# Kernel optimization log

Hardware: AMD Instinct MI355X
Metric: run time of the kernel (lower is better)

Reference implementation:

```python
import jax, jax.numpy as jnp
import numpy as np

IN_FEATURES = 4096
OUT_FEATURES = 4096
N_GROUPS = 32
GROUP_SIZE = IN_FEATURES // N_GROUPS  # 128


def setup_inputs() -> dict:
    key = jax.random.key(0)
    k_x, k_qw, k_s, k_zp, k_b = jax.random.split(key, 5)
    x = jax.random.normal(k_x, (2, 2048, IN_FEATURES), dtype=jnp.float32)
    # 4-bit GPTQ quantized weight values in [0, 16)
    qweight_int = jax.random.randint(k_qw, (IN_FEATURES, OUT_FEATURES), 0, 16, dtype=jnp.int32)
    scales = jax.random.uniform(k_s, (N_GROUPS, OUT_FEATURES), dtype=jnp.float32, minval=0.001, maxval=0.02)
    zero_points = jax.random.randint(k_zp, (N_GROUPS, OUT_FEATURES), 0, 16, dtype=jnp.int32)
    # standard (non-permuted) g_idx: group index per input channel
    g_idx = (jnp.arange(IN_FEATURES, dtype=jnp.int32) // GROUP_SIZE).astype(jnp.int32)
    bias = jax.random.normal(k_b, (OUT_FEATURES,), dtype=jnp.float32)
    return {"x": x, "qweight_int": qweight_int, "scales": scales,
            "zero_points": zero_points, "g_idx": g_idx, "bias": bias}


def reference(x, qweight_int, scales, zero_points, g_idx, bias):
    dtype = x.dtype
    gi = g_idx.astype(jnp.int32)
    # dequantize: W[i, o] = scales[g_idx[i], o] * (q[i, o] - zp[g_idx[i], o])
    qw = qweight_int.astype(dtype)                       # [in, out]
    zp = zero_points.astype(dtype)[gi]                   # [in, out] via gather
    sc = scales.astype(dtype)[gi]                        # [in, out] via gather
    weight = sc * (qw - zp)                              # [in, out]
    out_shape = x.shape[:-1] + (qweight_int.shape[1],)
    x2d = x.reshape(-1, x.shape[-1])                     # [tokens, in]
    out = (x2d @ weight).reshape(out_shape)              # [b, s, out]
    out = out + bias.astype(dtype)
    return out
```

## Files before the change

### kernel.cpp

```cpp
#include <hip/hip_runtime.h>
#include <hip/hip_bf16.h>

typedef int  int4v  __attribute__((ext_vector_type(4)));
typedef int  int16v __attribute__((ext_vector_type(16)));

#define M_DIM 4096
#define N_DIM 4096
#define K_DIM 4096
#define NG 32
#define GS 128

__global__ void prep_kernel(const float* __restrict__ x,
                            signed char* __restrict__ xq,
                            float* __restrict__ sx,
                            const int* __restrict__ qw,
                            const int* __restrict__ zps,
                            signed char* __restrict__ wq) {
    const int tid = threadIdx.x;
    if (blockIdx.x < 4096) {
        __shared__ float red[4];
        __shared__ float inv_s;
        const int m = blockIdx.x;
        const float4* xr = reinterpret_cast<const float4*>(x + (long)m * K_DIM);
        float4 v[4];
        float amax = 0.f;
#pragma unroll
        for (int j = 0; j < 4; ++j) {
            v[j] = xr[tid * 4 + j];
            amax = fmaxf(amax, fmaxf(fmaxf(fabsf(v[j].x), fabsf(v[j].y)),
                                     fmaxf(fabsf(v[j].z), fabsf(v[j].w))));
        }
#pragma unroll
        for (int off = 32; off >= 1; off >>= 1)
            amax = fmaxf(amax, __shfl_xor(amax, off));
        if ((tid & 63) == 0) red[tid >> 6] = amax;
        __syncthreads();
        if (tid == 0) {
            float a = fmaxf(fmaxf(red[0], red[1]), fmaxf(red[2], red[3]));
            sx[m] = a * (1.f / 127.f);
            inv_s = (a > 0.f) ? 127.f / a : 0.f;
        }
        __syncthreads();
        const float inv = inv_s;
        unsigned p[4];
#pragma unroll
        for (int j = 0; j < 4; ++j) {
            int a0 = __float2int_rn(v[j].x * inv);
            int a1 = __float2int_rn(v[j].y * inv);
            int a2 = __float2int_rn(v[j].z * inv);
            int a3 = __float2int_rn(v[j].w * inv);
            p[j] = (a0 & 255) | ((a1 & 255) << 8) | ((a2 & 255) << 16) | ((a3 & 255) << 24);
        }
        *reinterpret_cast<uint4*>(xq + (long)m * K_DIM + tid * 16) =
            make_uint4(p[0], p[1], p[2], p[3]);
        return;
    }
    __shared__ signed char lt[128 * 32];
    const int bx = blockIdx.x - 4096;
    const int n0 = (bx & 127) * 32;
    const int k0 = (bx >> 7) * 128;
    const int g  = bx >> 7;
    const int kl = tid >> 1;
    const int h  = tid & 1;
    int4 qv[4], zv[4];
#pragma unroll
    for (int c = 0; c < 4; ++c) {
        qv[c] = *reinterpret_cast<const int4*>(&qw[(long)(k0 + kl) * N_DIM + n0 + h * 16 + c * 4]);
        zv[c] = *reinterpret_cast<const int4*>(&zps[(long)g * N_DIM + n0 + h * 16 + c * 4]);
    }
    {
        const int swz = ((kl >> 3) & 7) << 2;
        int* ltw = reinterpret_cast<int*>(lt);
#pragma unroll
        for (int c = 0; c < 4; ++c) {
            unsigned d = (unsigned)((qv[c].x - zv[c].x) & 255)
                       | ((unsigned)((qv[c].y - zv[c].y) & 255) << 8)
                       | ((unsigned)((qv[c].z - zv[c].z) & 255) << 16)
                       | ((unsigned)((qv[c].w - zv[c].w) & 255) << 24);
            ltw[(kl * 32 + ((h * 16 + c * 4) ^ swz)) >> 2] = d;
        }
    }
    __syncthreads();
    const int nl = tid >> 3;
    const int kq = tid & 7;
    unsigned acc[4] = {0u, 0u, 0u, 0u};
#pragma unroll
    for (int j = 0; j < 16; ++j) {
        const int kr = kq * 16 + j;
        unsigned by = (unsigned char)lt[kr * 32 + (nl ^ (((kr >> 3) & 7) << 2))];
        acc[j >> 2] |= by << (8 * (j & 3));
    }
    *reinterpret_cast<uint4*>(wq + (long)(n0 + nl) * K_DIM + k0 + kq * 16) =
        make_uint4(acc[0], acc[1], acc[2], acc[3]);
}

#define BM 128
#define BN 256
#define BK 64
#define NSTEP (K_DIM / BK)

__device__ __forceinline__ void async_ld16(const signed char* g, const signed char* l) {
    __builtin_amdgcn_global_load_lds(
        (const __attribute__((address_space(1))) void*)g,
        (__attribute__((address_space(3))) void*)l, 16, 0, 0);
}

__device__ __forceinline__ int16v mf(const int4v a, const int4v b, const int16v c) {
    return __builtin_amdgcn_mfma_i32_32x32x32_i8(a, b, c, 0, 0, 0);
}

__device__ __forceinline__ int4v ld_frag(const signed char* buf, int row, int lu) {
    const int phys = lu ^ ((row >> 1) & 3);
    return *reinterpret_cast<const int4v*>(&buf[row * BK + phys * 16]);
}

__global__ __launch_bounds__(512, 4) void gemm_kernel(
    const signed char* __restrict__ A,
    const signed char* __restrict__ Bq,
    const float* __restrict__ scales,
    const float* __restrict__ sx,
    const float* __restrict__ bias,
    float* __restrict__ C) {
    __shared__ signed char As[2][BM * BK];
    __shared__ signed char Bs[2][BN * BK];
    const int tid  = threadIdx.x;
    const int wave = tid >> 6;
    const int lane = tid & 63;
    const int half = lane >> 5;
    const int l32  = lane & 31;
    const int wm = (wave >> 2) * 64;
    const int wn = (wave & 3) * 64;

    const int bid = (int)blockIdx.x;
    const int swz = (bid & 7) * 64 + (bid >> 3);
    const int m0 = (swz >> 4) * BM;
    const int n0 = (swz & 15) * BN;

    const int srow  = tid >> 2;
    const int sunit = (tid & 3) ^ ((tid >> 3) & 3);
    const signed char* agp = A  + (long)(m0 + srow) * K_DIM + sunit * 16;
    const signed char* bgp = Bq + (long)(n0 + srow) * K_DIM + sunit * 16;
    const float* sp = scales + n0 + wn + l32;

    float facc[2][2][16];
#pragma unroll
    for (int mt = 0; mt < 2; ++mt)
#pragma unroll
        for (int nt = 0; nt < 2; ++nt)
#pragma unroll
            for (int r = 0; r < 16; ++r) facc[mt][nt][r] = 0.f;
    int16v zero16;
#pragma unroll
    for (int r = 0; r < 16; ++r) zero16[r] = 0;

    async_ld16(agp,                      As[0] + wave * 1024);
    async_ld16(bgp,                      Bs[0] + wave * 1024);
    async_ld16(bgp + (long)128 * K_DIM,  Bs[0] + 8192 + wave * 1024);
    __syncthreads();

    float s0c = 0.f, s1c = 0.f;
    for (int t = 0; t < NSTEP; ++t) {
        const signed char* Ab = As[t & 1];
        const signed char* Bb = Bs[t & 1];
        if (t + 1 < NSTEP) {
            const long kn = (long)(t + 1) * BK;
            async_ld16(agp + kn,                     As[(t + 1) & 1] + wave * 1024);
            async_ld16(bgp + kn,                     Bs[(t + 1) & 1] + wave * 1024);
            async_ld16(bgp + (long)128 * K_DIM + kn, Bs[(t + 1) & 1] + 8192 + wave * 1024);
        }
        if ((t & 1) == 0) {
            s0c = sp[(long)(t >> 1) * N_DIM];
            s1c = sp[(long)(t >> 1) * N_DIM + 32];
        }
        int4v bf[2][2];
#pragma unroll
        for (int nt = 0; nt < 2; ++nt) {
            const int n = wn + nt * 32 + l32;
#pragma unroll
            for (int ks = 0; ks < 2; ++ks)
                bf[nt][ks] = ld_frag(Bb, n, 2 * ks + half);
        }
#pragma unroll
        for (int mt = 0; mt < 2; ++mt) {
            const int m = wm + mt * 32 + l32;
            int4v af[2];
#pragma unroll
            for (int ks = 0; ks < 2; ++ks)
                af[ks] = ld_frag(Ab, m, 2 * ks + half);
#pragma unroll
            for (int nt = 0; nt < 2; ++nt) {
                int16v c = mf(af[0], bf[nt][0], zero16);
                c = mf(af[1], bf[nt][1], c);
                const float s = nt ? s1c : s0c;
#pragma unroll
                for (int r = 0; r < 16; ++r)
                    facc[mt][nt][r] += s * (float)c[r];
            }
        }
        __syncthreads();
    }

    float bv[2];
    bv[0] = bias[n0 + wn + l32];
    bv[1] = bias[n0 + wn + 32 + l32];
    const int rowh = half * 4;
#pragma unroll
    for (int mt = 0; mt < 2; ++mt) {
#pragma unroll
        for (int r = 0; r < 16; ++r) {
            const int row = (r & 3) + 8 * (r >> 2) + rowh;
            const int gm  = m0 + wm + mt * 32 + row;
            const float sxm = sx[gm];
            float* crow = C + (long)gm * N_DIM + n0 + wn;
            crow[l32]      = facc[mt][0][r] * sxm + bv[0];
            crow[32 + l32] = facc[mt][1][r] * sxm + bv[1];
        }
    }
}

extern "C" void kernel_launch(void* const* d_in, const int* in_sizes, int n_in,
                              void* d_out, int out_size, void* d_ws, size_t ws_size,
                              hipStream_t stream) {
    const float* x      = (const float*)d_in[0];
    const int*   qw     = (const int*)d_in[1];
    const float* scales = (const float*)d_in[2];
    const int*   zps    = (const int*)d_in[3];
    const float* bias   = (const float*)d_in[5];
    float* out = (float*)d_out;

    signed char* xq = (signed char*)d_ws;
    signed char* wq = (signed char*)d_ws + (size_t)M_DIM * K_DIM;
    float*       sx = (float*)((signed char*)d_ws + 2 * (size_t)M_DIM * K_DIM);

    prep_kernel<<<8192, 256, 0, stream>>>(x, xq, sx, qw, zps, wq);
    gemm_kernel<<<(M_DIM / BM) * (N_DIM / BN), 512, 0, stream>>>(
        xq, wq, scales, sx, bias, out);
}
```

Before: 295.2 us.

## Restructure int8 GEMM to 128x128x128 tiles with 2 waves and single buffer

Rewrites the int8 MFMA GEMM to use 128x128 output tiles with BK=128 (one scale group per k-step), two waves per block each computing 128x64, and a single-buffered LDS with an 8-way XOR swizzle. The per-group float rescale now happens once per 128-k step instead of per 64-k chunk, and each wave computes more MFMAs per fragment load. It drops the double-buffered async prefetch, so global loads are no longer overlapped with compute within a block, and it relies on multiple resident blocks to hide latency instead.

```diff
diff --git a/kernel.cpp b/kernel.cpp
--- a/kernel.cpp
+++ b/kernel.cpp
@@ -95,9 +95,9 @@
 }
 
 #define BM 128
-#define BN 256
-#define BK 64
-#define NSTEP (K_DIM / BK)
+#define BN 128
+#define BK 128
+#define NT (K_DIM / BK)
 
 __device__ __forceinline__ void async_ld16(const signed char* g, const signed char* l) {
     __builtin_amdgcn_global_load_lds(
@@ -109,42 +109,36 @@
     return __builtin_amdgcn_mfma_i32_32x32x32_i8(a, b, c, 0, 0, 0);
 }
 
-__device__ __forceinline__ int4v ld_frag(const signed char* buf, int row, int lu) {
-    const int phys = lu ^ ((row >> 1) & 3);
-    return *reinterpret_cast<const int4v*>(&buf[row * BK + phys * 16]);
-}
-
-__global__ __launch_bounds__(512, 4) void gemm_kernel(
+__global__ __launch_bounds__(128, 2) void gemm_kernel(
     const signed char* __restrict__ A,
     const signed char* __restrict__ Bq,
     const float* __restrict__ scales,
     const float* __restrict__ sx,
     const float* __restrict__ bias,
     float* __restrict__ C) {
-    __shared__ signed char As[2][BM * BK];
-    __shared__ signed char Bs[2][BN * BK];
+    __shared__ signed char As[BM * BK];
+    __shared__ signed char Bs[BN * BK];
     const int tid  = threadIdx.x;
     const int wave = tid >> 6;
     const int lane = tid & 63;
     const int half = lane >> 5;
     const int l32  = lane & 31;
-    const int wm = (wave >> 2) * 64;
-    const int wn = (wave & 3) * 64;
+    const int wn = wave * 64;
 
     const int bid = (int)blockIdx.x;
-    const int swz = (bid & 7) * 64 + (bid >> 3);
-    const int m0 = (swz >> 4) * BM;
-    const int n0 = (swz & 15) * BN;
-
-    const int srow  = tid >> 2;
-    const int sunit = (tid & 3) ^ ((tid >> 3) & 3);
+    const int swz = (bid & 7) * 128 + (bid >> 3);
+    const int m0 = (swz >> 5) * BM;
+    const int n0 = (swz & 31) * BN;
+
+    const int srow  = tid >> 3;
+    const int sunit = (tid & 7) ^ (srow & 7);
     const signed char* agp = A  + (long)(m0 + srow) * K_DIM + sunit * 16;
     const signed char* bgp = Bq + (long)(n0 + srow) * K_DIM + sunit * 16;
     const float* sp = scales + n0 + wn + l32;
 
-    float facc[2][2][16];
-#pragma unroll
-    for (int mt = 0; mt < 2; ++mt)
+    float facc[4][2][16];
+#pragma unroll
+    for (int mt = 0; mt < 4; ++mt)
 #pragma unroll
         for (int nt = 0; nt < 2; ++nt)
 #pragma unroll
@@ -153,48 +147,47 @@
 #pragma unroll
     for (int r = 0; r < 16; ++r) zero16[r] = 0;
 
-    async_ld16(agp,                      As[0] + wave * 1024);
-    async_ld16(bgp,                      Bs[0] + wave * 1024);
-    async_ld16(bgp + (long)128 * K_DIM,  Bs[0] + 8192 + wave * 1024);
-    __syncthreads();
-
-    float s0c = 0.f, s1c = 0.f;
-    for (int t = 0; t < NSTEP; ++t) {
-        const signed char* Ab = As[t & 1];
-        const signed char* Bb = Bs[t & 1];
-        if (t + 1 < NSTEP) {
-            const long kn = (long)(t + 1) * BK;
-            async_ld16(agp + kn,                     As[(t + 1) & 1] + wave * 1024);
-            async_ld16(bgp + kn,                     Bs[(t + 1) & 1] + wave * 1024);
-            async_ld16(bgp + (long)128 * K_DIM + kn, Bs[(t + 1) & 1] + 8192 + wave * 1024);
-        }
-        if ((t & 1) == 0) {
-            s0c = sp[(long)(t >> 1) * N_DIM];
-            s1c = sp[(long)(t >> 1) * N_DIM + 32];
-        }
-        int4v bf[2][2];
+    for (int t = 0; t < NT; ++t) {
+        const long kk = (long)t * BK;
+#pragma unroll
+        for (int p = 0; p < 8; ++p) {
+            async_ld16(agp + (long)(p * 16) * K_DIM + kk, As + p * 2048 + wave * 1024);
+            async_ld16(bgp + (long)(p * 16) * K_DIM + kk, Bs + p * 2048 + wave * 1024);
+        }
+        __syncthreads();
+
+        const float s0 = sp[(long)t * N_DIM];
+        const float s1 = sp[(long)t * N_DIM + 32];
+        int4v bf[2][4];
 #pragma unroll
         for (int nt = 0; nt < 2; ++nt) {
             const int n = wn + nt * 32 + l32;
 #pragma unroll
-            for (int ks = 0; ks < 2; ++ks)
-                bf[nt][ks] = ld_frag(Bb, n, 2 * ks + half);
-        }
-#pragma unroll
-        for (int mt = 0; mt < 2; ++mt) {
-            const int m = wm + mt * 32 + l32;
-            int4v af[2];
-#pragma unroll
-            for (int ks = 0; ks < 2; ++ks)
-                af[ks] = ld_frag(Ab, m, 2 * ks + half);
-#pragma unroll
-            for (int nt = 0; nt < 2; ++nt) {
-                int16v c = mf(af[0], bf[nt][0], zero16);
-                c = mf(af[1], bf[nt][1], c);
-                const float s = nt ? s1c : s0c;
-#pragma unroll
-                for (int r = 0; r < 16; ++r)
-                    facc[mt][nt][r] += s * (float)c[r];
+            for (int ks = 0; ks < 4; ++ks) {
+                const int slot = (2 * ks + half) ^ (n & 7);
+                bf[nt][ks] = *reinterpret_cast<const int4v*>(&Bs[n * BK + slot * 16]);
+            }
+        }
+#pragma unroll
+        for (int mt = 0; mt < 4; ++mt) {
+            const int m = mt * 32 + l32;
+            int4v af[4];
+#pragma unroll
+            for (int ks = 0; ks < 4; ++ks) {
+                const int slot = (2 * ks + half) ^ (m & 7);
+                af[ks] = *reinterpret_cast<const int4v*>(&As[m * BK + slot * 16]);
+            }
+            int16v c0 = mf(af[0], bf[0][0], zero16);
+            int16v c1 = mf(af[0], bf[1][0], zero16);
+#pragma unroll
+            for (int ks = 1; ks < 4; ++ks) {
+                c0 = mf(af[ks], bf[0][ks], c0);
+                c1 = mf(af[ks], bf[1][ks], c1);
+            }
+#pragma unroll
+            for (int r = 0; r < 16; ++r) {
+                facc[mt][0][r] += s0 * (float)c0[r];
+                facc[mt][1][r] += s1 * (float)c1[r];
             }
         }
         __syncthreads();
@@ -205,11 +198,11 @@
     bv[1] = bias[n0 + wn + 32 + l32];
     const int rowh = half * 4;
 #pragma unroll
-    for (int mt = 0; mt < 2; ++mt) {
+    for (int mt = 0; mt < 4; ++mt) {
 #pragma unroll
         for (int r = 0; r < 16; ++r) {
             const int row = (r & 3) + 8 * (r >> 2) + rowh;
-            const int gm  = m0 + wm + mt * 32 + row;
+            const int gm  = m0 + mt * 32 + row;
             const float sxm = sx[gm];
             float* crow = C + (long)gm * N_DIM + n0 + wn;
             crow[l32]      = facc[mt][0][r] * sxm + bv[0];
@@ -233,6 +226,6 @@
     float*       sx = (float*)((signed char*)d_ws + 2 * (size_t)M_DIM * K_DIM);
 
     prep_kernel<<<8192, 256, 0, stream>>>(x, xq, sx, qw, zps, wq);
-    gemm_kernel<<<(M_DIM / BM) * (N_DIM / BN), 512, 0, stream>>>(
+    gemm_kernel<<<(M_DIM / BM) * (N_DIM / BN), 128, 0, stream>>>(
         xq, wq, scales, sx, bias, out);
 }
```

Result: faster. 268.9 us (-8.9%).
